# Kernel optimization log

Measured on AMD Instinct MI355X. Metric: run time of the kernel, lower is better.

Reference implementation:

```python
import jax, jax.numpy as jnp
import numpy as np

B, L, C = 8, 3136, 192
HEADS, HEAD_CH = 3, 64
EPS = 1e-5


def _dwconv(x, w, s):
    # depthwise 3x3 conv, SAME padding; w: [3,3,1,C], feature_group_count=C
    return jax.lax.conv_general_dilated(
        x, w, (s, s), 'SAME',
        dimension_numbers=('NHWC', 'HWIO', 'NHWC'),
        feature_group_count=x.shape[-1])


def _proj(x, dw, scale, bias, mean, var, pw, s):
    # depthwise conv -> BN (inference, running stats) -> 1x1 pointwise conv
    h = _dwconv(x, dw, s)
    h = (h - mean) * jax.lax.rsqrt(var + EPS) * scale + bias
    return jax.lax.conv_general_dilated(
        h, pw, (1, 1), 'SAME',
        dimension_numbers=('NHWC', 'HWIO', 'NHWC'))


def setup_inputs() -> dict:
    key = jax.random.key(0)
    ks = jax.random.split(key, 7)
    d = {'x': jax.random.normal(ks[0], (B, L, C), jnp.float32)}
    for i, p in enumerate(['q', 'k', 'v']):
        d[p + '_dw'] = jax.random.normal(ks[i + 1], (3, 3, 1, C), jnp.float32) * 0.1
        d[p + '_scale'] = jnp.ones((C,), jnp.float32)
        d[p + '_bias'] = jnp.zeros((C,), jnp.float32)
        d[p + '_mean'] = jnp.zeros((C,), jnp.float32)
        d[p + '_var'] = jnp.ones((C,), jnp.float32)
        d[p + '_pw'] = jax.random.normal(ks[i + 4], (1, 1, C, HEADS * HEAD_CH), jnp.float32) * 0.05
    d['is_training'] = 0  # inference: BN uses running averages
    return d


def reference(x, q_dw, q_scale, q_bias, q_mean, q_var, q_pw,
              k_dw, k_scale, k_bias, k_mean, k_var, k_pw,
              v_dw, v_scale, v_bias, v_mean, v_var, v_pw,
              is_training):
    S = int(np.ceil(np.sqrt(L)))  # 56; L is a perfect square, so no token padding
    xi = x.reshape(B, S, S, C)
    q = _proj(xi, q_dw, q_scale, q_bias, q_mean, q_var, q_pw, 1)  # [B,56,56,192]
    k = _proj(xi, k_dw, k_scale, k_bias, k_mean, k_var, k_pw, 2)  # [B,28,28,192]
    v = _proj(xi, v_dw, v_scale, v_bias, v_mean, v_var, v_pw, 2)  # [B,28,28,192]
    q = q.reshape(B, -1, HEADS, HEAD_CH) / jnp.sqrt(jnp.float32(HEAD_CH))
    k = k.reshape(B, -1, HEADS, HEAD_CH)
    v = v.reshape(B, -1, HEADS, HEAD_CH)
    attn = jax.nn.softmax(jnp.einsum('bqhd,bkhd->bhqk', q, k), axis=-1)
    o = jnp.einsum('bhqk,bkhd->bqhd', attn, v)
    # num_heads*head_ch == out_ch -> plain head merge, no output projection
    return o.reshape(B, L, HEADS * HEAD_CH)
```

## Files before the change

### kernel.cpp

```cpp
#include <hip/hip_runtime.h>
#include <cmath>

#define EPS_BN 1e-5f

typedef __bf16 bf16;
typedef __bf16 bf16x4 __attribute__((ext_vector_type(4)));
typedef __bf16 bf16x8 __attribute__((ext_vector_type(8)));
typedef float  f32x4  __attribute__((ext_vector_type(4)));

__device__ __forceinline__ void dma16(const bf16* g, bf16* l) {
    __builtin_amdgcn_global_load_lds(
        (const __attribute__((address_space(1))) void*)g,
        (__attribute__((address_space(3))) void*)l, 16, 0, 0);
}

__global__ __launch_bounds__(256) void conv_all_kernel(
    const float* __restrict__ x,
    const float* __restrict__ qdw, const float* __restrict__ qscale,
    const float* __restrict__ qbias, const float* __restrict__ qmean,
    const float* __restrict__ qvar,
    const float* __restrict__ kdw, const float* __restrict__ kscale,
    const float* __restrict__ kbias, const float* __restrict__ kmean,
    const float* __restrict__ kvar,
    const float* __restrict__ vdw, const float* __restrict__ vscale,
    const float* __restrict__ vbias, const float* __restrict__ vmean,
    const float* __restrict__ vvar,
    const float* __restrict__ qpw, const float* __restrict__ kpw,
    const float* __restrict__ vpw,
    bf16* __restrict__ qhi, bf16* __restrict__ qlo,
    bf16* __restrict__ khi, bf16* __restrict__ klo,
    bf16* __restrict__ vhi, bf16* __restrict__ vlo,
    bf16* __restrict__ wt) {
    const int WW = 56, C = 192;
    int bid = blockIdx.x;

    if (bid < 4704) {
        int idx = bid * 256 + threadIdx.x;
        int p  = idx / 48;
        int c4 = (idx - p * 48) * 4;
        int b  = p / 3136;
        int rem = p - b * 3136;
        int oy = rem / 56;
        int ox = rem - oy * 56;
        const float* xb = x + (size_t)b * 3136 * C;

        float4 sc = *(const float4*)&qscale[c4];
        float4 vr = *(const float4*)&qvar[c4];
        float4 bi = *(const float4*)&qbias[c4];
        float4 mn = *(const float4*)&qmean[c4];
        float aA[4] = {sc.x * rsqrtf(vr.x + EPS_BN), sc.y * rsqrtf(vr.y + EPS_BN),
                       sc.z * rsqrtf(vr.z + EPS_BN), sc.w * rsqrtf(vr.w + EPS_BN)};
        float aB[4] = {bi.x - mn.x * aA[0], bi.y - mn.y * aA[1],
                       bi.z - mn.z * aA[2], bi.w - mn.w * aA[3]};
        float s[4] = {0.f, 0.f, 0.f, 0.f};
#pragma unroll
        for (int ky = 0; ky < 3; ky++) {
            int iy = oy + ky - 1;
            bool yok = (iy >= 0) && (iy < 56);
#pragma unroll
            for (int kx = 0; kx < 3; kx++) {
                int ix = ox + kx - 1;
                if (yok && ix >= 0 && ix < WW) {
                    float4 xv = *(const float4*)&xb[((size_t)iy * WW + ix) * C + c4];
                    float4 wv = *(const float4*)&qdw[(ky * 3 + kx) * C + c4];
                    s[0] += xv.x * wv.x; s[1] += xv.y * wv.y;
                    s[2] += xv.z * wv.z; s[3] += xv.w * wv.w;
                }
            }
        }
        bf16x4 hv, lv;
#pragma unroll
        for (int j = 0; j < 4; j++) {
            float av = s[j] * aA[j] + aB[j];
            bf16 hh = (bf16)av;
            hv[j] = hh;
            lv[j] = (bf16)(av - (float)hh);
        }
        *(bf16x4*)&qhi[(size_t)p * C + c4] = hv;
        *(bf16x4*)&qlo[(size_t)p * C + c4] = lv;
    } else if (bid < 5880) {
        int idx = (bid - 4704) * 256 + threadIdx.x;
        int p  = idx / 48;
        int c4 = (idx - p * 48) * 4;
        int b  = p / 784;
        int rem = p - b * 784;
        int oy = rem / 28;
        int ox = rem - oy * 28;
        const float* xb = x + (size_t)b * 3136 * C;

        float ks[4] = {0.f, 0.f, 0.f, 0.f};
        float vs[4] = {0.f, 0.f, 0.f, 0.f};
#pragma unroll
        for (int ky = 0; ky < 3; ky++) {
            int iy = oy * 2 + ky;
            bool yok = iy < 56;
#pragma unroll
            for (int kx = 0; kx < 3; kx++) {
                int ix = ox * 2 + kx;
                if (yok && ix < WW) {
                    float4 xv = *(const float4*)&xb[((size_t)iy * WW + ix) * C + c4];
                    float4 kw = *(const float4*)&kdw[(ky * 3 + kx) * C + c4];
                    float4 vw = *(const float4*)&vdw[(ky * 3 + kx) * C + c4];
                    ks[0] += xv.x * kw.x; ks[1] += xv.y * kw.y;
                    ks[2] += xv.z * kw.z; ks[3] += xv.w * kw.w;
                    vs[0] += xv.x * vw.x; vs[1] += xv.y * vw.y;
                    vs[2] += xv.z * vw.z; vs[3] += xv.w * vw.w;
                }
            }
        }
        float4 ksc = *(const float4*)&kscale[c4];
        float4 kvr = *(const float4*)&kvar[c4];
        float4 kbi = *(const float4*)&kbias[c4];
        float4 kmn = *(const float4*)&kmean[c4];
        float4 vsc = *(const float4*)&vscale[c4];
        float4 vvr = *(const float4*)&vvar[c4];
        float4 vbi = *(const float4*)&vbias[c4];
        float4 vmn = *(const float4*)&vmean[c4];
        float kA[4] = {ksc.x * rsqrtf(kvr.x + EPS_BN), ksc.y * rsqrtf(kvr.y + EPS_BN),
                       ksc.z * rsqrtf(kvr.z + EPS_BN), ksc.w * rsqrtf(kvr.w + EPS_BN)};
        float kB[4] = {kbi.x - kmn.x * kA[0], kbi.y - kmn.y * kA[1],
                       kbi.z - kmn.z * kA[2], kbi.w - kmn.w * kA[3]};
        float vA[4] = {vsc.x * rsqrtf(vvr.x + EPS_BN), vsc.y * rsqrtf(vvr.y + EPS_BN),
                       vsc.z * rsqrtf(vvr.z + EPS_BN), vsc.w * rsqrtf(vvr.w + EPS_BN)};
        float vB[4] = {vbi.x - vmn.x * vA[0], vbi.y - vmn.y * vA[1],
                       vbi.z - vmn.z * vA[2], vbi.w - vmn.w * vA[3]};
        bf16x4 kh, kl, vh, vl;
#pragma unroll
        for (int j = 0; j < 4; j++) {
            float kf = ks[j] * kA[j] + kB[j];
            float vf = vs[j] * vA[j] + vB[j];
            bf16 h1 = (bf16)kf; kh[j] = h1; kl[j] = (bf16)(kf - (float)h1);
            bf16 h2 = (bf16)vf; vh[j] = h2; vl[j] = (bf16)(vf - (float)h2);
        }
        *(bf16x4*)&khi[(size_t)p * C + c4] = kh;
        *(bf16x4*)&klo[(size_t)p * C + c4] = kl;
        *(bf16x4*)&vhi[(size_t)p * C + c4] = vh;
        *(bf16x4*)&vlo[(size_t)p * C + c4] = vl;
    } else {
        int idx = (bid - 5880) * 256 + threadIdx.x;
        if (idx < 3 * 36864) {
            int mat = idx / 36864, r = idx % 36864;
            int n = r / 192, k = r - n * 192;
            const float* src = (mat == 0) ? qpw : (mat == 1) ? kpw : vpw;
            wt[idx] = (bf16)src[k * 192 + n];
        }
    }
}

__global__ __launch_bounds__(256) void gemm_all_kernel(
    const bf16* __restrict__ qhi, const bf16* __restrict__ qlo,
    const bf16* __restrict__ khi, const bf16* __restrict__ klo,
    const bf16* __restrict__ vhi, const bf16* __restrict__ vlo,
    const bf16* __restrict__ wt,
    bf16* __restrict__ qbuf, bf16* __restrict__ kbuf, bf16* __restrict__ vtbuf) {
    __shared__ bf16 Ws[192][200];
    int t = threadIdx.x;
    int bid = blockIdx.x;

    int mode, mt;
    const bf16 *Ahi, *Alo, *Wsrc;
    if (bid < 392)      { mode = 0; mt = bid;       Ahi = qhi; Alo = qlo; Wsrc = wt; }
    else if (bid < 490) { mode = 1; mt = bid - 392; Ahi = khi; Alo = klo; Wsrc = wt + 36864; }
    else                { mode = 2; mt = bid - 490; Ahi = vhi; Alo = vlo; Wsrc = wt + 73728; }

#pragma unroll
    for (int it = 0; it < 18; it++) {
        int idx = it * 256 + t;
        int n = idx / 24, ck = idx - n * 24;
        *(uint4*)&Ws[n][ck * 8] = *(const uint4*)&Wsrc[n * 192 + ck * 8];
    }
    __syncthreads();

    int lane = t & 63, wid = t >> 6;
    int l16 = lane & 15, quad = lane >> 4;
    int wrow = wid * 16;
    int m0 = mt * 64;

    f32x4 acc[12];
#pragma unroll
    for (int n = 0; n < 12; n++) acc[n] = f32x4{0.f, 0.f, 0.f, 0.f};

    const bf16* arh = Ahi + (size_t)(m0 + wrow + l16) * 192;
    const bf16* arl = Alo + (size_t)(m0 + wrow + l16) * 192;
#pragma unroll
    for (int kc = 0; kc < 6; kc++) {
        bf16x8 ah = *(const bf16x8*)(arh + kc * 32 + quad * 8);
        bf16x8 al = *(const bf16x8*)(arl + kc * 32 + quad * 8);
#pragma unroll
        for (int n = 0; n < 12; n++) {
            bf16x8 bfr = *(const bf16x8*)&Ws[n * 16 + l16][kc * 32 + quad * 8];
            acc[n] = __builtin_amdgcn_mfma_f32_16x16x32_bf16(al, bfr, acc[n], 0, 0, 0);
            acc[n] = __builtin_amdgcn_mfma_f32_16x16x32_bf16(ah, bfr, acc[n], 0, 0, 0);
        }
    }

    if (mode == 2) {
#pragma unroll
        for (int reg = 0; reg < 4; reg++) {
            int row = m0 + wrow + quad * 4 + reg;
            int b = row / 784;
            int loc = row - b * 784;
#pragma unroll
            for (int n = 0; n < 12; n++) {
                int col = n * 16 + l16;
                int h = col >> 6, d = col & 63;
                vtbuf[(((size_t)b * 3 + h) * 64 + d) * 784 + loc] = (bf16)acc[n][reg];
            }
        }
    } else {
        bf16* outp = (mode == 0) ? qbuf : kbuf;
        const float s = (mode == 0) ? 0.18033688f : 1.0f;
#pragma unroll
        for (int reg = 0; reg < 4; reg++) {
            size_t row = m0 + wrow + quad * 4 + reg;
#pragma unroll
            for (int n = 0; n < 12; n++)
                outp[row * 192 + n * 16 + l16] = (bf16)(acc[n][reg] * s);
        }
    }
}

__global__ __launch_bounds__(256)
__attribute__((amdgpu_waves_per_eu(3, 3)))
void attn6_kernel(const bf16* __restrict__ qb,
                  const bf16* __restrict__ kb,
                  const bf16* __restrict__ vtb,
                  float* __restrict__ out) {
    const int LQ = 3136, LK = 784, C = 192;
    int qp = blockIdx.x;
    int h  = blockIdx.y, b = blockIdx.z;
    bool tile1_valid = (qp < 24);

    __shared__ bf16 Ks[8192];
    __shared__ bf16 Vts[64][136];
    __shared__ bf16 Ps[64][136];

    int t    = threadIdx.x;
    int lane = t & 63;
    int wid  = t >> 6;
    int l16  = lane & 15;
    int quad = lane >> 4;
    int wrow = wid * 16;

    if (t < 128) {
        int row = t >> 1, part = t & 1;
        *(uint4*)&Ps[row][112 + part * 8] = make_uint4(0u, 0u, 0u, 0u);
    }

    bf16x8 qfrag[2][2];
#pragma unroll
    for (int tl = 0; tl < 2; tl++) {
        int tloff = (tl == 1 && tile1_valid) ? 64 : 0;
        int row = qp * 128 + tloff + wrow + l16;
        const bf16* qrow = qb + ((size_t)b * LQ + row) * C + h * 64;
        qfrag[tl][0] = *(const bf16x8*)(qrow + quad * 8);
        qfrag[tl][1] = *(const bf16x8*)(qrow + 32 + quad * 8);
    }

    const bf16* kbase  = kb + (size_t)b * LK * C + h * 64;
    const bf16* vtbase = vtb + ((size_t)(b * 3 + h)) * 64 * LK;

    float m_run[2] = {-INFINITY, -INFINITY};
    float l_run[2] = {0.f, 0.f};
    f32x4 o_acc[2][4];
#pragma unroll
    for (int tl = 0; tl < 2; tl++)
#pragma unroll
        for (int dt = 0; dt < 4; dt++) o_acc[tl][dt] = f32x4{0.f, 0.f, 0.f, 0.f};

    for (int c = 0; c < 7; c++) {
        int j0 = c * 112;
        __syncthreads();

        for (int s = wid; s < 33; s += 4) {
            if (s < 16) {
                int j = s * 64 + lane;
                int r = j / 9, cc = j - r * 9;
                const bf16* src = (cc < 8 && r < 112)
                                  ? kbase + (size_t)(j0 + r) * C + cc * 8
                                  : kbase;
                dma16(src, &Ks[s * 512]);
            } else {
                int s2 = s - 16;
                int j = s2 * 64 + lane;
                int r = j / 17, cc = j - r * 17;
                const bf16* src = (cc < 14)
                                  ? vtbase + (size_t)r * LK + j0 + cc * 8
                                  : vtbase;
                dma16(src, (bf16*)Vts + s2 * 512);
            }
        }
        __syncthreads();

#pragma unroll
        for (int tl = 0; tl < 2; tl++) {
            f32x4 st[7];
#pragma unroll
            for (int kb7 = 0; kb7 < 7; kb7++) st[kb7] = f32x4{0.f, 0.f, 0.f, 0.f};
#pragma unroll
            for (int kk = 0; kk < 2; kk++) {
#pragma unroll
                for (int kb7 = 0; kb7 < 7; kb7++) {
                    bf16x8 afrag = *(const bf16x8*)&Ks[(kb7 * 16 + l16) * 72 + kk * 32 + quad * 8];
                    st[kb7] = __builtin_amdgcn_mfma_f32_16x16x32_bf16(afrag, qfrag[tl][kk], st[kb7], 0, 0, 0);
                }
            }

            float mx = -INFINITY;
#pragma unroll
            for (int kb7 = 0; kb7 < 7; kb7++)
#pragma unroll
                for (int r = 0; r < 4; r++) mx = fmaxf(mx, st[kb7][r]);
            mx = fmaxf(mx, __shfl_xor(mx, 16, 64));
            mx = fmaxf(mx, __shfl_xor(mx, 32, 64));
            float m_new = fmaxf(m_run[tl], mx);
            float alpha = exp2f(m_run[tl] - m_new);

            float rs = 0.f;
#pragma unroll
            for (int kb7 = 0; kb7 < 7; kb7++) {
                bf16x4 pv;
#pragma unroll
                for (int r = 0; r < 4; r++) {
                    float p = exp2f(st[kb7][r] - m_new);
                    rs += p;
                    pv[r] = (bf16)p;
                }
                *(bf16x4*)&Ps[wrow + l16][kb7 * 16 + quad * 4] = pv;
            }
            rs += __shfl_xor(rs, 16, 64);
            rs += __shfl_xor(rs, 32, 64);
            l_run[tl] = l_run[tl] * alpha + rs;
            m_run[tl] = m_new;
#pragma unroll
            for (int dt = 0; dt < 4; dt++)
#pragma unroll
                for (int r = 0; r < 4; r++) o_acc[tl][dt][r] *= alpha;

#pragma unroll
            for (int kk = 0; kk < 4; kk++) {
                bf16x8 pfrag = *(const bf16x8*)&Ps[wrow + l16][kk * 32 + quad * 8];
#pragma unroll
                for (int dt = 0; dt < 4; dt++) {
                    bf16x8 vfrag = *(const bf16x8*)&Vts[dt * 16 + l16][kk * 32 + quad * 8];
                    o_acc[tl][dt] = __builtin_amdgcn_mfma_f32_16x16x32_bf16(vfrag, pfrag, o_acc[tl][dt], 0, 0, 0);
                }
            }
        }
    }

#pragma unroll
    for (int tl = 0; tl < 2; tl++) {
        if (tl == 1 && !tile1_valid) break;
        float invl = 1.f / l_run[tl];
        float* ob = out + ((size_t)b * LQ + qp * 128 + tl * 64 + wrow + l16) * C + h * 64;
#pragma unroll
        for (int dt = 0; dt < 4; dt++) {
            float4 v4 = {o_acc[tl][dt][0] * invl, o_acc[tl][dt][1] * invl,
                         o_acc[tl][dt][2] * invl, o_acc[tl][dt][3] * invl};
            *(float4*)(ob + dt * 16 + quad * 4) = v4;
        }
    }
}

extern "C" void kernel_launch(void* const* d_in, const int* in_sizes, int n_in,
                              void* d_out, int out_size, void* d_ws, size_t ws_size,
                              hipStream_t stream) {
    const float* x = (const float*)d_in[0];

    const float* q_dw = (const float*)d_in[1];
    const float* q_scale = (const float*)d_in[2];
    const float* q_bias = (const float*)d_in[3];
    const float* q_mean = (const float*)d_in[4];
    const float* q_var = (const float*)d_in[5];
    const float* q_pw = (const float*)d_in[6];

    const float* k_dw = (const float*)d_in[7];
    const float* k_scale = (const float*)d_in[8];
    const float* k_bias = (const float*)d_in[9];
    const float* k_mean = (const float*)d_in[10];
    const float* k_var = (const float*)d_in[11];
    const float* k_pw = (const float*)d_in[12];

    const float* v_dw = (const float*)d_in[13];
    const float* v_scale = (const float*)d_in[14];
    const float* v_bias = (const float*)d_in[15];
    const float* v_mean = (const float*)d_in[16];
    const float* v_var = (const float*)d_in[17];
    const float* v_pw = (const float*)d_in[18];

    float* out = (float*)d_out;

    char* ws = (char*)d_ws;
    bf16* qhi = (bf16*)(ws);
    bf16* qlo = (bf16*)(ws + 9633792);
    bf16* khi = (bf16*)(ws + 19267584);
    bf16* klo = (bf16*)(ws + 21676032);
    bf16* vhi = (bf16*)(ws + 24084480);
    bf16* vlo = (bf16*)(ws + 26492928);
    bf16* qbuf = (bf16*)(ws + 28901376);
    bf16* kbuf = (bf16*)(ws + 38535168);
    bf16* vtbuf = (bf16*)(ws + 40943616);
    bf16* wt = (bf16*)(ws + 43352064);

    conv_all_kernel<<<6312, 256, 0, stream>>>(
        x,
        q_dw, q_scale, q_bias, q_mean, q_var,
        k_dw, k_scale, k_bias, k_mean, k_var,
        v_dw, v_scale, v_bias, v_mean, v_var,
        q_pw, k_pw, v_pw,
        qhi, qlo, khi, klo, vhi, vlo, wt);

    gemm_all_kernel<<<588, 256, 0, stream>>>(
        qhi, qlo, khi, klo, vhi, vlo, wt, qbuf, kbuf, vtbuf);

    attn6_kernel<<<dim3(25, 3, 8), 256, 0, stream>>>(qbuf, kbuf, vtbuf, out);
}
```

Measured before the change: 191.9 us.

## Double-buffer K/V chunk loads in attention kernel to overlap DMA with compute

The attention kernel now prefetches the next K and V^T chunk into a second LDS buffer via direct global-to-LDS DMA while computing on the current chunk, with one barrier per iteration instead of two. LDS row strides are changed (K 72→80, V/P 136→144) and the occupancy hint drops from 3 to 1 wave per EU, since the larger LDS footprint limits blocks per CU anyway. The trade is overlap of memory latency against lower occupancy. Correctness depends on the LDS DMA completing before the end-of-iteration barrier.

```diff
diff --git a/kernel.cpp b/kernel.cpp
--- a/kernel.cpp
+++ b/kernel.cpp
@@ -221,8 +221,8 @@
 }
 
 __global__ __launch_bounds__(256)
-__attribute__((amdgpu_waves_per_eu(3, 3)))
-void attn6_kernel(const bf16* __restrict__ qb,
+__attribute__((amdgpu_waves_per_eu(1, 1)))
+void attn7_kernel(const bf16* __restrict__ qb,
                   const bf16* __restrict__ kb,
                   const bf16* __restrict__ vtb,
                   float* __restrict__ out) {
@@ -231,9 +231,9 @@
     int h  = blockIdx.y, b = blockIdx.z;
     bool tile1_valid = (qp < 24);
 
-    __shared__ bf16 Ks[8192];
-    __shared__ bf16 Vts[64][136];
-    __shared__ bf16 Ps[64][136];
+    __shared__ bf16 Ks2[2][9216];
+    __shared__ bf16 Vts2[2][9216];
+    __shared__ bf16 Ps[9216];
 
     int t    = threadIdx.x;
     int lane = t & 63;
@@ -244,7 +244,7 @@
 
     if (t < 128) {
         int row = t >> 1, part = t & 1;
-        *(uint4*)&Ps[row][112 + part * 8] = make_uint4(0u, 0u, 0u, 0u);
+        *(uint4*)&Ps[row * 144 + 112 + part * 8] = make_uint4(0u, 0u, 0u, 0u);
     }
 
     bf16x8 qfrag[2][2];
@@ -260,6 +260,29 @@
     const bf16* kbase  = kb + (size_t)b * LK * C + h * 64;
     const bf16* vtbase = vtb + ((size_t)(b * 3 + h)) * 64 * LK;
 
+    auto issue_chunk = [&](int j0, int buf) {
+#pragma unroll
+        for (int i = 0; i < 9; i++) {
+            int s = wid * 9 + i;
+            if (s < 18) {
+                int j = s * 64 + lane;
+                int r = j / 10, cc = j - r * 10;
+                const bf16* src = (cc < 8 && r < 112)
+                                  ? kbase + (size_t)(j0 + r) * C + cc * 8
+                                  : kbase;
+                dma16(src, &Ks2[buf][s * 512]);
+            } else {
+                int s2 = s - 18;
+                int j = s2 * 64 + lane;
+                int r = j / 18, cc = j - r * 18;
+                const bf16* src = (cc < 14)
+                                  ? vtbase + (size_t)r * LK + j0 + cc * 8
+                                  : vtbase;
+                dma16(src, &Vts2[buf][s2 * 512]);
+            }
+        }
+    };
+
     float m_run[2] = {-INFINITY, -INFINITY};
     float l_run[2] = {0.f, 0.f};
     f32x4 o_acc[2][4];
@@ -268,29 +291,15 @@
 #pragma unroll
         for (int dt = 0; dt < 4; dt++) o_acc[tl][dt] = f32x4{0.f, 0.f, 0.f, 0.f};
 
+    issue_chunk(0, 0);
+    __syncthreads();
+
     for (int c = 0; c < 7; c++) {
-        int j0 = c * 112;
-        __syncthreads();
-
-        for (int s = wid; s < 33; s += 4) {
-            if (s < 16) {
-                int j = s * 64 + lane;
-                int r = j / 9, cc = j - r * 9;
-                const bf16* src = (cc < 8 && r < 112)
-                                  ? kbase + (size_t)(j0 + r) * C + cc * 8
-                                  : kbase;
-                dma16(src, &Ks[s * 512]);
-            } else {
-                int s2 = s - 16;
-                int j = s2 * 64 + lane;
-                int r = j / 17, cc = j - r * 17;
-                const bf16* src = (cc < 14)
-                                  ? vtbase + (size_t)r * LK + j0 + cc * 8
-                                  : vtbase;
-                dma16(src, (bf16*)Vts + s2 * 512);
-            }
-        }
-        __syncthreads();
+        int cb = c & 1;
+        if (c < 6) issue_chunk((c + 1) * 112, cb ^ 1);
+
+        const bf16* KsB  = Ks2[cb];
+        const bf16* VtsB = Vts2[cb];
 
 #pragma unroll
         for (int tl = 0; tl < 2; tl++) {
@@ -301,7 +310,7 @@
             for (int kk = 0; kk < 2; kk++) {
 #pragma unroll
                 for (int kb7 = 0; kb7 < 7; kb7++) {
-                    bf16x8 afrag = *(const bf16x8*)&Ks[(kb7 * 16 + l16) * 72 + kk * 32 + quad * 8];
+                    bf16x8 afrag = *(const bf16x8*)&KsB[(kb7 * 16 + l16) * 80 + kk * 32 + quad * 8];
                     st[kb7] = __builtin_amdgcn_mfma_f32_16x16x32_bf16(afrag, qfrag[tl][kk], st[kb7], 0, 0, 0);
                 }
             }
@@ -326,7 +335,7 @@
                     rs += p;
                     pv[r] = (bf16)p;
                 }
-                *(bf16x4*)&Ps[wrow + l16][kb7 * 16 + quad * 4] = pv;
+                *(bf16x4*)&Ps[(wrow + l16) * 144 + kb7 * 16 + quad * 4] = pv;
             }
             rs += __shfl_xor(rs, 16, 64);
             rs += __shfl_xor(rs, 32, 64);
@@ -339,14 +348,16 @@
 
 #pragma unroll
             for (int kk = 0; kk < 4; kk++) {
-                bf16x8 pfrag = *(const bf16x8*)&Ps[wrow + l16][kk * 32 + quad * 8];
+                bf16x8 pfrag = *(const bf16x8*)&Ps[(wrow + l16) * 144 + kk * 32 + quad * 8];
 #pragma unroll
                 for (int dt = 0; dt < 4; dt++) {
-                    bf16x8 vfrag = *(const bf16x8*)&Vts[dt * 16 + l16][kk * 32 + quad * 8];
+                    bf16x8 vfrag = *(const bf16x8*)&VtsB[(dt * 16 + l16) * 144 + kk * 32 + quad * 8];
                     o_acc[tl][dt] = __builtin_amdgcn_mfma_f32_16x16x32_bf16(vfrag, pfrag, o_acc[tl][dt], 0, 0, 0);
                 }
             }
         }
+
+        __syncthreads();
     }
 
 #pragma unroll
@@ -414,5 +425,5 @@
     gemm_all_kernel<<<588, 256, 0, stream>>>(
         qhi, qlo, khi, klo, vhi, vlo, wt, qbuf, kbuf, vtbuf);
 
-    attn6_kernel<<<dim3(25, 3, 8), 256, 0, stream>>>(qbuf, kbuf, vtbuf, out);
+    attn7_kernel<<<dim3(25, 3, 8), 256, 0, stream>>>(qbuf, kbuf, vtbuf, out);
 }
```

Measured after the change: 221.1 us. +15.2%, slower.
